# Kernel optimization log

Measured on AMD Instinct MI355X. Metric: run time of the kernel, lower is better.

## Reference

```python
import jax, jax.numpy as jnp
import numpy as np

B, T, H, W, C = 2, 8, 32, 32, 192
DI, N, K, DTR = 384, 16, 4, 12   # d_inner=2*dim, d_state, scan directions, dt_rank=ceil(dim/16)
LT, HID = 77, 768
L = T * H * W


def setup_inputs() -> dict:
    key = jax.random.key(0)
    ks = jax.random.split(key, 16)
    r = lambda i, shape, s=1.0: jax.random.normal(ks[i], shape, dtype=jnp.float32) * s
    return {
        "x": r(0, (B, T, H, W, C)),
        "text": r(1, (B, LT, C)),
        "cpe1_w": r(2, (C, 1, 3, 3, 3), 0.05), "cpe1_b": jnp.zeros((C,), jnp.float32),
        "cpe2_w": r(3, (C, 1, 3, 3, 3), 0.05), "cpe2_b": jnp.zeros((C,), jnp.float32),
        "norm1_g": jnp.ones((C,), jnp.float32), "norm1_b": jnp.zeros((C,), jnp.float32),
        "norm2_g": jnp.ones((C,), jnp.float32), "norm2_b": jnp.zeros((C,), jnp.float32),
        "in_proj_w": r(4, (2 * DI, C), 0.02), "in_proj_b": jnp.zeros((2 * DI,), jnp.float32),
        "text_proj_w": r(5, (DI, C), 0.02), "text_proj_b": jnp.zeros((DI,), jnp.float32),
        "conv_w": r(6, (DI, 1, 3, 3, 3), 0.05), "conv_b": jnp.zeros((DI,), jnp.float32),
        "x_proj_w": r(7, (K, DTR + 2 * N, DI), 0.02),
        "dt_proj_w": r(8, (K, DI, DTR), 0.1), "dt_proj_b": r(9, (K, DI), 0.1),
        "A_log": jnp.log(jnp.tile(jnp.arange(1.0, N + 1.0, dtype=jnp.float32)[None, None, :], (K, DI, 1))),
        "Ds": jnp.ones((K, DI), jnp.float32),
        "out_norm_g": jnp.ones((DI,), jnp.float32), "out_norm_b": jnp.zeros((DI,), jnp.float32),
        "out_proj_w": r(10, (C, DI), 0.02),
        "fc1_w": r(11, (HID, C), 0.02), "fc1_b": jnp.zeros((HID,), jnp.float32),
        "fc2_w": r(12, (C, HID), 0.02), "fc2_b": jnp.zeros((C,), jnp.float32),
    }


def _ln(x, g, b, eps=1e-6):
    m = x.mean(-1, keepdims=True)
    v = jnp.mean((x - m) ** 2, -1, keepdims=True)
    return (x - m) * jax.lax.rsqrt(v + eps) * g + b


def _dwconv3d(x, w, b):  # x [B, Ch, T, H, W], depthwise 3x3x3, SAME padding
    y = jax.lax.conv_general_dilated(x, w, (1, 1, 1), 'SAME',
                                     feature_group_count=x.shape[1],
                                     dimension_numbers=('NCDHW', 'OIDHW', 'NCDHW'))
    return y + b[None, :, None, None, None]


def _cpe(x, w, b):  # conv positional encoding, channels-last in/out
    return jnp.transpose(_dwconv3d(jnp.transpose(x, (0, 4, 1, 2, 3)), w, b), (0, 2, 3, 4, 1))


def _ss2d(x, text, p):
    # in-projection -> (x, z) gate split
    xz = x @ p['in_proj_w'].T + p['in_proj_b']           # [B,T,H,W,2*DI]
    xi, z = jnp.split(xz, 2, axis=-1)
    # text conditioning (pooled text tokens -> channel bias)
    cond = jax.nn.silu(text.mean(1) @ p['text_proj_w'].T + p['text_proj_b'])  # [B,DI]
    xi = xi + cond[:, None, None, None, :]
    # depthwise conv3d + SiLU
    xc = jax.nn.silu(_dwconv3d(jnp.transpose(xi, (0, 4, 1, 2, 3)), p['conv_w'], p['conv_b']))  # [B,DI,T,H,W]
    # cross-scan: (t,h,w), (t,w,h) and their reversals
    x0 = xc.reshape(B, DI, L)
    x1 = jnp.swapaxes(xc, 3, 4).reshape(B, DI, L)
    xs = jnp.stack([x0, x1, jnp.flip(x0, -1), jnp.flip(x1, -1)], 1)  # [B,K,DI,L]
    # per-direction projections
    xdbl = jnp.einsum('bkdl,kcd->bkcl', xs, p['x_proj_w'])
    dtr, Bm, Cm = jnp.split(xdbl, [DTR, DTR + N], axis=2)            # [B,K,DTR,L],[B,K,N,L],[B,K,N,L]
    dt = jax.nn.softplus(jnp.einsum('bkrl,kdr->bkdl', dtr, p['dt_proj_w']) + p['dt_proj_b'][None, :, :, None])
    A = -jnp.exp(p['A_log'])                                          # [K,DI,N]
    def step(h, inp):
        u_l, dt_l, B_l, C_l = inp
        h = h * jnp.exp(dt_l[..., None] * A) + (dt_l * u_l)[..., None] * B_l[:, :, None, :]
        return h, jnp.einsum('bkdn,bkn->bkd', h, C_l)
    seq = (xs.transpose(3, 0, 1, 2), dt.transpose(3, 0, 1, 2),
           Bm.transpose(3, 0, 1, 2), Cm.transpose(3, 0, 1, 2))
    _, ys = jax.lax.scan(step, jnp.zeros((B, K, DI, N), xs.dtype), seq)  # ys [L,B,K,DI]
    ys = ys.transpose(1, 2, 3, 0) + p['Ds'][None, :, :, None] * xs       # [B,K,DI,L]
    # merge the 4 directions back into (t,h,w) order
    unt = lambda y: jnp.swapaxes(y.reshape(B, DI, T, W, H), 3, 4).reshape(B, DI, L)
    y = ys[:, 0] + jnp.flip(ys[:, 2], -1) + unt(ys[:, 1]) + unt(jnp.flip(ys[:, 3], -1))
    y = _ln(y.transpose(0, 2, 1), p['out_norm_g'], p['out_norm_b']).reshape(B, T, H, W, DI)
    y = y * jax.nn.silu(z)
    return y @ p['out_proj_w'].T


def reference(x, text, cpe1_w, cpe1_b, cpe2_w, cpe2_b, norm1_g, norm1_b, norm2_g, norm2_b,
              in_proj_w, in_proj_b, text_proj_w, text_proj_b, conv_w, conv_b,
              x_proj_w, dt_proj_w, dt_proj_b, A_log, Ds, out_norm_g, out_norm_b, out_proj_w,
              fc1_w, fc1_b, fc2_w, fc2_b):
    p = dict(in_proj_w=in_proj_w, in_proj_b=in_proj_b, text_proj_w=text_proj_w,
             text_proj_b=text_proj_b, conv_w=conv_w, conv_b=conv_b, x_proj_w=x_proj_w,
             dt_proj_w=dt_proj_w, dt_proj_b=dt_proj_b, A_log=A_log, Ds=Ds,
             out_norm_g=out_norm_g, out_norm_b=out_norm_b, out_proj_w=out_proj_w)
    x = x + _cpe(x, cpe1_w, cpe1_b)
    x = x + _ss2d(_ln(x, norm1_g, norm1_b), text, p)
    x = x + _cpe(x, cpe2_w, cpe2_b)
    h = _ln(x, norm2_g, norm2_b)
    x = x + (jax.nn.gelu(h @ fc1_w.T + fc1_b) @ fc2_w.T + fc2_b)
    return x
```

## Files before the change

kernel.cpp:

```cpp
#include <hip/hip_runtime.h>
#include <hip/hip_bf16.h>

#define DEV __device__ __forceinline__

namespace {

constexpr int cB = 2, cT = 8, cH = 32, cW = 32, cC = 192;
constexpr int cDI = 384, cN = 16, cK = 4, cDTR = 12, cLT = 77, cHID = 768;
constexpr int cL  = cT * cH * cW;
constexpr int cBL = cB * cL;
constexpr int SEG = 128, SEGLEN = cL / SEG;
constexpr int XROW = cDTR + 2 * cN;
constexpr int XSTR = 48;

typedef __attribute__((ext_vector_type(8))) short bf16x8;
typedef __attribute__((ext_vector_type(4))) float f32x4;
typedef __attribute__((ext_vector_type(4))) short short4v;

DEV float bfu2f(unsigned short u) { return __uint_as_float(((unsigned)u) << 16); }
DEV float ldsel(const void* p, size_t i, int f32) {
  return f32 ? ((const float*)p)[i] : bfu2f(((const unsigned short*)p)[i]);
}
template <int F32>
DEV float4 ld4(const void* p, size_t e) {
  if (F32) return *(const float4*)((const float*)p + e);
  ushort4 u = *(const ushort4*)((const unsigned short*)p + e);
  return make_float4(bfu2f(u.x), bfu2f(u.y), bfu2f(u.z), bfu2f(u.w));
}
DEV short f2bf(float f) {
  unsigned u = __float_as_uint(f);
  u += 0x7fffu + ((u >> 16) & 1u);
  return (short)(u >> 16);
}
DEV float siluf(float x) { return x / (1.f + __expf(-x)); }
DEV float softplusf(float x) { return (x > 20.f) ? x : __logf(1.f + __expf(x)); }
DEV float gelut(float x) {
  float u = 0.7978845608028654f * (x + 0.044715f * x * x * x);
  float e = __expf(2.f * u);
  float th = 1.f - 2.f / (e + 1.f);
  return 0.5f * x * (1.f + th);
}

template <int BS>
DEV void blkreduce2(float& a, float& b) {
  __shared__ float ra[BS], rb[BS];
  int t = threadIdx.x;
  ra[t] = a; rb[t] = b; __syncthreads();
#pragma unroll
  for (int s = BS / 2; s > 0; s >>= 1) {
    if (t < s) { ra[t] += ra[t + s]; rb[t] += rb[t + s]; }
    __syncthreads();
  }
  a = ra[0]; b = rb[0];
  __syncthreads();
}

__global__ void __launch_bounds__(256) detect_kernel(
    const unsigned short* __restrict__ xa, const unsigned short* __restrict__ wp,
    int* __restrict__ flg) {
  __shared__ int cnt[2];
  if (threadIdx.x < 2) cnt[threadIdx.x] = 0;
  __syncthreads();
  int l0 = 0, l1 = 0;
  for (int i = threadIdx.x; i < 1024; i += 256) {
    float v = bfu2f(xa[2 * i]); float a = fabsf(v);
    if (v == 0.f || (a > 1e-8f && a < 1e4f)) l0++;
    float u = bfu2f(wp[2 * i]); float bq = fabsf(u);
    if (u == 0.f || (bq > 1e-8f && bq < 1e4f)) l1++;
  }
  atomicAdd(&cnt[0], l0); atomicAdd(&cnt[1], l1);
  __syncthreads();
  if (threadIdx.x == 0) {
    flg[0] = (cnt[0] < 614) ? 1 : 0;
    flg[1] = (cnt[1] < 614) ? 1 : 0;
    flg[2] = 1;
  }
}

__global__ void __launch_bounds__(256) prep_kernel(
    const void* __restrict__ cvw, const void* __restrict__ cvb,
    const void* __restrict__ c1w, const void* __restrict__ c1b,
    const void* __restrict__ c2w, const void* __restrict__ c2b,
    const int* __restrict__ flg,
    float* __restrict__ wcv, float* __restrict__ bcv,
    float* __restrict__ w1, float* __restrict__ b1,
    float* __restrict__ w2, float* __restrict__ b2) {
  int pf = flg[1];
  int i = blockIdx.x * 256 + threadIdx.x;
  int r = i;
  if (r < 27 * cDI) { int j = r / cDI, d = r % cDI; wcv[r] = ldsel(cvw, (size_t)d * 27 + j, pf); return; }
  r -= 27 * cDI;
  if (r < cDI) { bcv[r] = ldsel(cvb, r, pf); return; }
  r -= cDI;
  if (r < 27 * cC) { int j = r / cC, c = r % cC; w1[r] = ldsel(c1w, (size_t)c * 27 + j, pf); return; }
  r -= 27 * cC;
  if (r < cC) { b1[r] = ldsel(c1b, r, pf); return; }
  r -= cC;
  if (r < 27 * cC) { int j = r / cC, c = r % cC; w2[r] = ldsel(c2w, (size_t)c * 27 + j, pf); return; }
  r -= 27 * cC;
  if (r < cC) { b2[r] = ldsel(c2b, r, pf); return; }
}

template <int F32>
DEV void cpe_body(const void* __restrict__ xin, const float* __restrict__ wT,
                  const float* __restrict__ bs, int idx, float* __restrict__ out) {
  int c = (idx % (cC / 4)) * 4; int bv = idx / (cC / 4);
  int v = bv & (cL - 1); int b = bv >> 13;
  int t = v >> 10, q = v & 1023, h = q >> 5, w = q & 31;
  float4 acc = *(const float4*)(bs + c);
#pragma unroll
  for (int dz = 0; dz < 3; ++dz) {
    int tt = t + dz - 1; if ((unsigned)tt >= (unsigned)cT) continue;
#pragma unroll
    for (int dy = 0; dy < 3; ++dy) {
      int hh = h + dy - 1; if ((unsigned)hh >= (unsigned)cH) continue;
#pragma unroll
      for (int dx = 0; dx < 3; ++dx) {
        int ww = w + dx - 1; if ((unsigned)ww >= (unsigned)cW) continue;
        int vv = (tt << 10) + (hh << 5) + ww;
        float4 wv = *(const float4*)(wT + (dz * 9 + dy * 3 + dx) * cC + c);
        float4 xv = ld4<F32>(xin, ((size_t)b * cL + vv) * cC + c);
        acc.x += wv.x * xv.x; acc.y += wv.y * xv.y;
        acc.z += wv.z * xv.z; acc.w += wv.w * xv.w;
      }
    }
  }
  float4 x0 = ld4<F32>(xin, (size_t)bv * cC + c);
  float4 o = make_float4(x0.x + acc.x, x0.y + acc.y, x0.z + acc.z, x0.w + acc.w);
  *(float4*)(out + (size_t)bv * cC + c) = o;
}

__global__ void __launch_bounds__(256) cpe_kernel(
    const void* __restrict__ xin, const float* __restrict__ wT,
    const float* __restrict__ bs, const int* __restrict__ flg, int afidx,
    float* __restrict__ out) {
  int idx = blockIdx.x * 256 + threadIdx.x;
  if (idx >= cBL * cC / 4) return;
  if (flg[afidx]) cpe_body<1>(xin, wT, bs, idx, out);
  else            cpe_body<0>(xin, wT, bs, idx, out);
}

__global__ void __launch_bounds__(256) dwconv_silu_kernel(
    const float* __restrict__ xin, const float* __restrict__ wT,
    const float* __restrict__ bs, unsigned short* __restrict__ out) {
  int idx = blockIdx.x * 256 + threadIdx.x;
  if (idx >= cBL * cDI / 4) return;
  int d = (idx % (cDI / 4)) * 4; int bv = idx / (cDI / 4);
  int v = bv & (cL - 1); int b = bv >> 13;
  int t = v >> 10, q = v & 1023, h = q >> 5, w = q & 31;
  float4 acc = *(const float4*)(bs + d);
#pragma unroll
  for (int dz = 0; dz < 3; ++dz) {
    int tt = t + dz - 1; if ((unsigned)tt >= (unsigned)cT) continue;
#pragma unroll
    for (int dy = 0; dy < 3; ++dy) {
      int hh = h + dy - 1; if ((unsigned)hh >= (unsigned)cH) continue;
#pragma unroll
      for (int dx = 0; dx < 3; ++dx) {
        int ww = w + dx - 1; if ((unsigned)ww >= (unsigned)cW) continue;
        int vv = (tt << 10) + (hh << 5) + ww;
        float4 wv = *(const float4*)(wT + (dz * 9 + dy * 3 + dx) * cDI + d);
        float4 xv = *(const float4*)(xin + ((size_t)b * cL + vv) * cDI + d);
        acc.x += wv.x * xv.x; acc.y += wv.y * xv.y;
        acc.z += wv.z * xv.z; acc.w += wv.w * xv.w;
      }
    }
  }
  ushort4 o;
  o.x = (unsigned short)f2bf(siluf(acc.x));
  o.y = (unsigned short)f2bf(siluf(acc.y));
  o.z = (unsigned short)f2bf(siluf(acc.z));
  o.w = (unsigned short)f2bf(siluf(acc.w));
  *(ushort4*)(out + (size_t)bv * cDI + d) = o;
}

__global__ void __launch_bounds__(256) ln_kernel(
    const float* __restrict__ in, const void* __restrict__ g,
    const void* __restrict__ bb, const int* __restrict__ flg,
    float* __restrict__ out, int D) {
  int pf = flg[1];
  int row = blockIdx.x;
  const float* x = in + (size_t)row * D;
  float s1 = 0.f, s2 = 0.f;
  for (int i = threadIdx.x; i < D; i += 256) { float v = x[i]; s1 += v; s2 += v * v; }
  blkreduce2<256>(s1, s2);
  float mean = s1 / D;
  float var = s2 / D - mean * mean;
  float rstd = rsqrtf(var + 1e-6f);
  float* o = out + (size_t)row * D;
  for (int i = threadIdx.x; i < D; i += 256)
    o[i] = (x[i] - mean) * rstd * ldsel(g, i, pf) + ldsel(bb, i, pf);
}

__global__ void __launch_bounds__(384) text_cond_kernel(
    const void* __restrict__ text, const void* __restrict__ tw,
    const void* __restrict__ tb, const int* __restrict__ flg,
    float* __restrict__ cond) {
  int af = flg[0], pf = flg[1];
  __shared__ float mean[cC];
  int b = blockIdx.x;
  for (int c = threadIdx.x; c < cC; c += 384) {
    float s = 0.f;
    for (int t = 0; t < cLT; ++t) s += ldsel(text, ((size_t)b * cLT + t) * cC + c, af);
    mean[c] = s * (1.f / cLT);
  }
  __syncthreads();
  int di = threadIdx.x;
  float a = ldsel(tb, di, pf);
  for (int c = 0; c < cC; ++c) a += mean[c] * ldsel(tw, di * cC + c, pf);
  cond[b * cDI + di] = siluf(a);
}

template <int MODE, int ABF>
__global__ void __launch_bounds__(256) gemm_mfma_kernel(
    const void* __restrict__ A, const void* __restrict__ W,
    int N, int K, const void* __restrict__ bias, const int* __restrict__ flg,
    const float* __restrict__ extra, float* __restrict__ out,
    unsigned short* __restrict__ out2) {
  constexpr int BM = 128, BN = 64, BK = 32, PK = 40;
  __shared__ short As[BM * PK];
  __shared__ short Bs[BN * PK];
  int pf = flg[1];
  int tid = threadIdx.x;
  int m0 = blockIdx.y * BM, n0 = blockIdx.x * BN;
  int lane = tid & 63, wv = tid >> 6;
  int wm = (wv >> 1) * 64, wn = (wv & 1) * 32;
  int lr = lane & 15, quad = lane >> 4;
  f32x4 acc[4][2];
#pragma unroll
  for (int mi = 0; mi < 4; ++mi)
#pragma unroll
    for (int ni = 0; ni < 2; ++ni) { acc[mi][ni][0]=0.f; acc[mi][ni][1]=0.f; acc[mi][ni][2]=0.f; acc[mi][ni][3]=0.f; }
  int ar = tid >> 1, aks = (tid & 1) * 16;
  int wr = tid >> 2, wks = (tid & 3) * 8;
  for (int k0 = 0; k0 < K; k0 += BK) {
    if (ABF) {
      const unsigned short* ap = (const unsigned short*)A + (size_t)(m0 + ar) * K + k0 + aks;
      short* da = &As[ar * PK + aks];
#pragma unroll
      for (int i = 0; i < 4; ++i)
        *(short4v*)(da + i * 4) = *(const short4v*)(ap + i * 4);
    } else {
      const float* ap = (const float*)A + (size_t)(m0 + ar) * K + k0 + aks;
      short* da = &As[ar * PK + aks];
#pragma unroll
      for (int i = 0; i < 4; ++i) {
        float4 v = ((const float4*)ap)[i];
        short4v h; h.x = f2bf(v.x); h.y = f2bf(v.y); h.z = f2bf(v.z); h.w = f2bf(v.w);
        *(short4v*)(da + i * 4) = h;
      }
    }
    {
      int nr = n0 + wr;
      short hb[8];
      if (nr < N) {
        size_t wi = (size_t)nr * K + k0 + wks;
        if (pf) {
#pragma unroll
          for (int i = 0; i < 8; ++i) hb[i] = f2bf(((const float*)W)[wi + i]);
        } else {
#pragma unroll
          for (int i = 0; i < 8; ++i) hb[i] = (short)((const unsigned short*)W)[wi + i];
        }
      } else {
#pragma unroll
        for (int i = 0; i < 8; ++i) hb[i] = 0;
      }
      short* db = &Bs[wr * PK + wks];
#pragma unroll
      for (int i = 0; i < 8; i += 4) {
        short4v h; h.x = hb[i]; h.y = hb[i+1]; h.z = hb[i+2]; h.w = hb[i+3];
        *(short4v*)(db + i) = h;
      }
    }
    __syncthreads();
    bf16x8 af[4], bfr[2];
#pragma unroll
    for (int mi = 0; mi < 4; ++mi)
      af[mi] = *(const bf16x8*)&As[(wm + mi * 16 + lr) * PK + quad * 8];
#pragma unroll
    for (int ni = 0; ni < 2; ++ni)
      bfr[ni] = *(const bf16x8*)&Bs[(wn + ni * 16 + lr) * PK + quad * 8];
#pragma unroll
    for (int mi = 0; mi < 4; ++mi)
#pragma unroll
      for (int ni = 0; ni < 2; ++ni)
        acc[mi][ni] = __builtin_amdgcn_mfma_f32_16x16x32_bf16(af[mi], bfr[ni], acc[mi][ni], 0, 0, 0);
    __syncthreads();
  }
#pragma unroll
  for (int mi = 0; mi < 4; ++mi) {
#pragma unroll
    for (int ni = 0; ni < 2; ++ni) {
#pragma unroll
      for (int r = 0; r < 4; ++r) {
        int m = m0 + wm + mi * 16 + quad * 4 + r;
        int n = n0 + wn + ni * 16 + lr;
        float v = acc[mi][ni][r];
        if (MODE == 0) {
          float bvv = ldsel(bias, n, pf);
          int b = m >> 13;
          if (n < cDI) out[(size_t)m * cDI + n] = v + bvv + extra[b * cDI + n];
          else         out2[(size_t)m * cDI + (n - cDI)] = (unsigned short)f2bf(v + bvv);
        } else if (MODE == 1) {
          if (n < cK * XROW) {
            int k = n / XROW, c = n - k * XROW;
            int b = m >> 13, vv = m & (cL - 1);
            int t = vv >> 10, q = vv & 1023, h = q >> 5, w = q & 31;
            int l1 = (t << 10) + (w << 5) + h;
            int lk = (k == 0) ? vv : (k == 1) ? l1 : (k == 2) ? (cL - 1 - vv) : (cL - 1 - l1);
            out[((size_t)(b * cK + k) * cL + lk) * XSTR + c] = v;
          }
        } else if (MODE == 2) {
          out[(size_t)m * cC + n] = v + extra[(size_t)m * cC + n];
        } else if (MODE == 3) {
          out[(size_t)m * cHID + n] = gelut(v + ldsel(bias, n, pf));
        } else {
          out[(size_t)m * cC + n] = v + ldsel(bias, n, pf) + extra[(size_t)m * cC + n];
        }
      }
    }
  }
}

DEV int scan_voxel(int k, int l) {
  if (k == 0) return l;
  if (k == 2) return cL - 1 - l;
  int ll = (k == 1) ? l : (cL - 1 - l);
  int t = ll >> 10, q = ll & 1023, w = q >> 5, h = q & 31;
  return (t << 10) + (h << 5) + w;
}

struct Row11 { float4 r0, r1, r2, r3, r4, r5, r6, r7, r8, r9, r10; };
struct Row7  { float4 r0, r1, r2, r7, r8, r9, r10; };

DEV Row11 ldrow11(const float* __restrict__ rows, int st) {
  const float4* rp = (const float4*)(rows + st * XSTR);
  Row11 q;
  q.r0 = rp[0]; q.r1 = rp[1]; q.r2 = rp[2]; q.r3 = rp[3]; q.r4 = rp[4];
  q.r5 = rp[5]; q.r6 = rp[6]; q.r7 = rp[7]; q.r8 = rp[8]; q.r9 = rp[9];
  q.r10 = rp[10];
  return q;
}
DEV Row7 ldrow7(const float* __restrict__ rows, int st) {
  const float4* rp = (const float4*)(rows + st * XSTR);
  Row7 q;
  q.r0 = rp[0]; q.r1 = rp[1]; q.r2 = rp[2];
  q.r7 = rp[7]; q.r8 = rp[8]; q.r9 = rp[9]; q.r10 = rp[10];
  return q;
}

DEV float s1step(const Row11& q, float u,
                 const float (&wdt)[cDTR], float dtb, float ac0, float Dsd,
                 float (&h)[cN], float& P1) {
  float s0 = dtb + q.r0.x*wdt[0] + q.r0.z*wdt[2] + q.r1.x*wdt[4] + q.r1.z*wdt[6] + q.r2.x*wdt[8] + q.r2.z*wdt[10];
  float s1 = q.r0.y*wdt[1] + q.r0.w*wdt[3] + q.r1.y*wdt[5] + q.r1.w*wdt[7] + q.r2.y*wdt[9] + q.r2.w*wdt[11];
  float dt = softplusf(s0 + s1);
  float a1 = exp2f(dt * ac0);
  float a2 = a1*a1, a3 = a2*a1, a4 = a2*a2;
  float a5 = a4*a1, a6 = a4*a2, a7 = a4*a3, a8 = a4*a4;
  float a9 = a8*a1, a10 = a8*a2, a11 = a8*a3, a12 = a8*a4;
  float a13 = a8*a5, a14 = a8*a6, a15 = a8*a7, a16 = a8*a8;
  float dtu = dt * u;
  P1 *= a1;
  float yp0 = Dsd * u, yp1 = 0.f, yp2 = 0.f, yp3 = 0.f;
  h[0]  = h[0] *a1  + dtu*q.r3.x; yp0 += h[0] *q.r7.x;
  h[1]  = h[1] *a2  + dtu*q.r3.y; yp1 += h[1] *q.r7.y;
  h[2]  = h[2] *a3  + dtu*q.r3.z; yp2 += h[2] *q.r7.z;
  h[3]  = h[3] *a4  + dtu*q.r3.w; yp3 += h[3] *q.r7.w;
  h[4]  = h[4] *a5  + dtu*q.r4.x; yp0 += h[4] *q.r8.x;
  h[5]  = h[5] *a6  + dtu*q.r4.y; yp1 += h[5] *q.r8.y;
  h[6]  = h[6] *a7  + dtu*q.r4.z; yp2 += h[6] *q.r8.z;
  h[7]  = h[7] *a8  + dtu*q.r4.w; yp3 += h[7] *q.r8.w;
  h[8]  = h[8] *a9  + dtu*q.r5.x; yp0 += h[8] *q.r9.x;
  h[9]  = h[9] *a10 + dtu*q.r5.y; yp1 += h[9] *q.r9.y;
  h[10] = h[10]*a11 + dtu*q.r5.z; yp2 += h[10]*q.r9.z;
  h[11] = h[11]*a12 + dtu*q.r5.w; yp3 += h[11]*q.r9.w;
  h[12] = h[12]*a13 + dtu*q.r6.x; yp0 += h[12]*q.r10.x;
  h[13] = h[13]*a14 + dtu*q.r6.y; yp1 += h[13]*q.r10.y;
  h[14] = h[14]*a15 + dtu*q.r6.z; yp2 += h[14]*q.r10.z;
  h[15] = h[15]*a16 + dtu*q.r6.w; yp3 += h[15]*q.r10.w;
  return (yp0 + yp1) + (yp2 + yp3);
}

DEV float s3step(const Row7& q,
                 const float (&wdt)[cDTR], float dtb, float ac0,
                 float (&g)[cN]) {
  float s0 = dtb + q.r0.x*wdt[0] + q.r0.z*wdt[2] + q.r1.x*wdt[4] + q.r1.z*wdt[6] + q.r2.x*wdt[8] + q.r2.z*wdt[10];
  float s1 = q.r0.y*wdt[1] + q.r0.w*wdt[3] + q.r1.y*wdt[5] + q.r1.w*wdt[7] + q.r2.y*wdt[9] + q.r2.w*wdt[11];
  float dt = softplusf(s0 + s1);
  float a1 = exp2f(dt * ac0);
  float a2 = a1*a1, a3 = a2*a1, a4 = a2*a2;
  float a5 = a4*a1, a6 = a4*a2, a7 = a4*a3, a8 = a4*a4;
  float a9 = a8*a1, a10 = a8*a2, a11 = a8*a3, a12 = a8*a4;
  float a13 = a8*a5, a14 = a8*a6, a15 = a8*a7, a16 = a8*a8;
  float yp0 = 0.f, yp1 = 0.f, yp2 = 0.f, yp3 = 0.f;
  g[0]  *= a1;  yp0 += g[0] *q.r7.x;
  g[1]  *= a2;  yp1 += g[1] *q.r7.y;
  g[2]  *= a3;  yp2 += g[2] *q.r7.z;
  g[3]  *= a4;  yp3 += g[3] *q.r7.w;
  g[4]  *= a5;  yp0 += g[4] *q.r8.x;
  g[5]  *= a6;  yp1 += g[5] *q.r8.y;
  g[6]  *= a7;  yp2 += g[6] *q.r8.z;
  g[7]  *= a8;  yp3 += g[7] *q.r8.w;
  g[8]  *= a9;  yp0 += g[8] *q.r9.x;
  g[9]  *= a10; yp1 += g[9] *q.r9.y;
  g[10] *= a11; yp2 += g[10]*q.r9.z;
  g[11] *= a12; yp3 += g[11]*q.r9.w;
  g[12] *= a13; yp0 += g[12]*q.r10.x;
  g[13] *= a14; yp1 += g[13]*q.r10.y;
  g[14] *= a15; yp2 += g[14]*q.r10.z;
  g[15] *= a16; yp3 += g[15]*q.r10.w;
  return (yp0 + yp1) + (yp2 + yp3);
}

__global__ void __launch_bounds__(128, 3) scan1_kernel(
    const unsigned short* __restrict__ xch, const float* __restrict__ xdbl,
    const void* __restrict__ dtw, const void* __restrict__ dtbv,
    const void* __restrict__ alog, const void* __restrict__ dsv,
    const int* __restrict__ flg,
    unsigned short* __restrict__ ys0, unsigned short* __restrict__ ys1,
    unsigned short* __restrict__ ys2, unsigned short* __restrict__ ys3,
    unsigned short* __restrict__ hend, unsigned short* __restrict__ pend) {
  __shared__ float rows[SEGLEN * XSTR];
  int pf = flg[1];
  int tid = threadIdx.x;
  int d = blockIdx.x * 128 + tid;
  int bks = blockIdx.y;
  int s = bks & (SEG - 1); int bk = bks / SEG; int k = bk & 3; int b = bk >> 2;
  int l0 = s * SEGLEN;
  {
    const float4* src = (const float4*)(xdbl + ((size_t)bk * cL + l0) * XSTR);
    float4* dst = (float4*)rows;
#pragma unroll
    for (int i = 0; i < (SEGLEN * XSTR / 4) / 128; ++i)
      dst[tid + i * 128] = src[tid + i * 128];
  }
  float wdt[cDTR];
#pragma unroll
  for (int r = 0; r < cDTR; ++r) wdt[r] = ldsel(dtw, (size_t)(k * cDI + d) * cDTR + r, pf);
  float dtb = ldsel(dtbv, k * cDI + d, pf);
  float ac[cN];
#pragma unroll
  for (int n = 0; n < cN; ++n)
    ac[n] = -__expf(ldsel(alog, (size_t)(k * cDI + d) * cN + n, pf)) * 1.4426950408889634f;
  bool fast = true;
#pragma unroll
  for (int n = 1; n < cN; ++n)
    fast = fast && (fabsf(ac[n] - (float)(n + 1) * ac[0]) <= 1e-3f * fabsf(ac[n]));
  float Dsd = ldsel(dsv, k * cDI + d, pf);
  float h[cN];
#pragma unroll
  for (int n = 0; n < cN; ++n) h[n] = 0.f;
  size_t so = ((size_t)bks * cDI + d) * cN;
  const unsigned short* xcb = xch + (size_t)b * cL * cDI + d;
  unsigned short* ysk = (k == 0) ? ys0 : (k == 1) ? ys1 : (k == 2) ? ys2 : ys3;
  unsigned short* ysrow = ysk + ((size_t)b * cL + l0) * cDI + d;
  __syncthreads();
  if (fast) {
    float ac0 = ac[0];
    float P1 = 1.f;
    Row11 qa = ldrow11(rows, 0);
    float u0 = bfu2f(xcb[(size_t)scan_voxel(k, l0) * cDI]);
    float u1 = bfu2f(xcb[(size_t)scan_voxel(k, l0 + 1) * cDI]);
    for (int st = 0; st < SEGLEN; st += 2) {
      Row11 qb = ldrow11(rows, st + 1);
      int p2 = (st + 2 < SEGLEN) ? st + 2 : SEGLEN - 1;
      int p3 = (st + 3 < SEGLEN) ? st + 3 : SEGLEN - 1;
      float nu0 = bfu2f(xcb[(size_t)scan_voxel(k, l0 + p2) * cDI]);
      float nu1 = bfu2f(xcb[(size_t)scan_voxel(k, l0 + p3) * cDI]);
      float ya = s1step(qa, u0, wdt, dtb, ac0, Dsd, h, P1);
      ysrow[(size_t)st * cDI] = (unsigned short)f2bf(ya);
      qa = ldrow11(rows, p2);
      float yb = s1step(qb, u1, wdt, dtb, ac0, Dsd, h, P1);
      ysrow[(size_t)(st + 1) * cDI] = (unsigned short)f2bf(yb);
      u0 = nu0; u1 = nu1;
    }
    float pp = P1;
#pragma unroll
    for (int n = 0; n < cN; ++n) {
      hend[so + n] = (unsigned short)f2bf(h[n]);
      pend[so + n] = (unsigned short)f2bf(pp);
      pp *= P1;
    }
  } else {
    float P[cN];
#pragma unroll
    for (int n = 0; n < cN; ++n) P[n] = 1.f;
    for (int st = 0; st < SEGLEN; ++st) {
      int l = l0 + st;
      const float4* rp = (const float4*)(rows + st * XSTR);
      float4 q0 = rp[0], q1 = rp[1], q2 = rp[2];
      float s0 = dtb + q0.x*wdt[0] + q0.z*wdt[2] + q1.x*wdt[4] + q1.z*wdt[6] + q2.x*wdt[8] + q2.z*wdt[10];
      float s1 = q0.y*wdt[1] + q0.w*wdt[3] + q1.y*wdt[5] + q1.w*wdt[7] + q2.y*wdt[9] + q2.w*wdt[11];
      float dt = softplusf(s0 + s1);
      float Bv[cN], Cv[cN];
      float4 qb0 = rp[3], qb1 = rp[4], qb2 = rp[5], qb3 = rp[6];
      float4 qc0 = rp[7], qc1 = rp[8], qc2 = rp[9], qc3 = rp[10];
      Bv[0]=qb0.x; Bv[1]=qb0.y; Bv[2]=qb0.z; Bv[3]=qb0.w;
      Bv[4]=qb1.x; Bv[5]=qb1.y; Bv[6]=qb1.z; Bv[7]=qb1.w;
      Bv[8]=qb2.x; Bv[9]=qb2.y; Bv[10]=qb2.z; Bv[11]=qb2.w;
      Bv[12]=qb3.x; Bv[13]=qb3.y; Bv[14]=qb3.z; Bv[15]=qb3.w;
      Cv[0]=qc0.x; Cv[1]=qc0.y; Cv[2]=qc0.z; Cv[3]=qc0.w;
      Cv[4]=qc1.x; Cv[5]=qc1.y; Cv[6]=qc1.z; Cv[7]=qc1.w;
      Cv[8]=qc2.x; Cv[9]=qc2.y; Cv[10]=qc2.z; Cv[11]=qc2.w;
      Cv[12]=qc3.x; Cv[13]=qc3.y; Cv[14]=qc3.z; Cv[15]=qc3.w;
      int v = scan_voxel(k, l);
      float u = bfu2f(xcb[(size_t)v * cDI]);
      float dtu = dt * u;
      float y = Dsd * u;
#pragma unroll
      for (int n = 0; n < cN; ++n) {
        float a = exp2f(dt * ac[n]);
        h[n] = h[n] * a + dtu * Bv[n];
        P[n] *= a;
        y += h[n] * Cv[n];
      }
      ysrow[(size_t)st * cDI] = (unsigned short)f2bf(y);
    }
#pragma unroll
    for (int n = 0; n < cN; ++n) {
      hend[so + n] = (unsigned short)f2bf(h[n]);
      pend[so + n] = (unsigned short)f2bf(P[n]);
    }
  }
}

__global__ void __launch_bounds__(256) scan2_kernel(
    unsigned short* __restrict__ hend, const unsigned short* __restrict__ pend) {
  int tid = blockIdx.x * 256 + threadIdx.x;
  int bk = tid / (cDI * cN); int r = tid - bk * (cDI * cN);
  float g = 0.f;
  for (int s = 0; s < SEG; ++s) {
    size_t o = ((size_t)(bk * SEG + s) * cDI * cN) + r;
    float he = bfu2f(hend[o]), pe = bfu2f(pend[o]);
    hend[o] = (unsigned short)f2bf(g);
    g = pe * g + he;
  }
}

__global__ void __launch_bounds__(128, 3) scan3_kernel(
    const float* __restrict__ xdbl,
    const void* __restrict__ dtw, const void* __restrict__ dtbv,
    const void* __restrict__ alog, const int* __restrict__ flg,
    const unsigned short* __restrict__ hin,
    unsigned short* __restrict__ ys0, unsigned short* __restrict__ ys1,
    unsigned short* __restrict__ ys2, unsigned short* __restrict__ ys3) {
  int bks = blockIdx.y;
  int s = bks & (SEG - 1);
  if (s == 0) return;
  __shared__ float rows[SEGLEN * XSTR];
  int pf = flg[1];
  int tid = threadIdx.x;
  int d = blockIdx.x * 128 + tid;
  int bk = bks / SEG; int k = bk & 3; int b = bk >> 2;
  int l0 = s * SEGLEN;
  {
    const float4* src = (const float4*)(xdbl + ((size_t)bk * cL + l0) * XSTR);
    float4* dst = (float4*)rows;
#pragma unroll
    for (int i = 0; i < (SEGLEN * XSTR / 4) / 128; ++i)
      dst[tid + i * 128] = src[tid + i * 128];
  }
  float wdt[cDTR];
#pragma unroll
  for (int r = 0; r < cDTR; ++r) wdt[r] = ldsel(dtw, (size_t)(k * cDI + d) * cDTR + r, pf);
  float dtb = ldsel(dtbv, k * cDI + d, pf);
  float ac[cN];
#pragma unroll
  for (int n = 0; n < cN; ++n)
    ac[n] = -__expf(ldsel(alog, (size_t)(k * cDI + d) * cN + n, pf)) * 1.4426950408889634f;
  bool fast = true;
#pragma unroll
  for (int n = 1; n < cN; ++n)
    fast = fast && (fabsf(ac[n] - (float)(n + 1) * ac[0]) <= 1e-3f * fabsf(ac[n]));
  float g[cN];
  size_t so = ((size_t)bks * cDI + d) * cN;
#pragma unroll
  for (int n = 0; n < cN; ++n) g[n] = bfu2f(hin[so + n]);
  unsigned short* ysk = (k == 0) ? ys0 : (k == 1) ? ys1 : (k == 2) ? ys2 : ys3;
  unsigned short* ysrow = ysk + ((size_t)b * cL + l0) * cDI + d;
  __syncthreads();
  if (fast) {
    float ac0 = ac[0];
    Row7 qa = ldrow7(rows, 0);
    for (int st = 0; st < SEGLEN; st += 2) {
      Row7 qb = ldrow7(rows, st + 1);
      int p2 = (st + 2 < SEGLEN) ? st + 2 : SEGLEN - 1;
      float ya = s3step(qa, wdt, dtb, ac0, g);
      size_t ia = (size_t)st * cDI;
      ysrow[ia] = (unsigned short)f2bf(bfu2f(ysrow[ia]) + ya);
      qa = ldrow7(rows, p2);
      float yb = s3step(qb, wdt, dtb, ac0, g);
      size_t ib = (size_t)(st + 1) * cDI;
      ysrow[ib] = (unsigned short)f2bf(bfu2f(ysrow[ib]) + yb);
    }
  } else {
    for (int st = 0; st < SEGLEN; ++st) {
      const float4* rp = (const float4*)(rows + st * XSTR);
      float4 q0 = rp[0], q1 = rp[1], q2 = rp[2];
      float s0 = dtb + q0.x*wdt[0] + q0.z*wdt[2] + q1.x*wdt[4] + q1.z*wdt[6] + q2.x*wdt[8] + q2.z*wdt[10];
      float s1 = q0.y*wdt[1] + q0.w*wdt[3] + q1.y*wdt[5] + q1.w*wdt[7] + q2.y*wdt[9] + q2.w*wdt[11];
      float dt = softplusf(s0 + s1);
      float Cv[cN];
      float4 qc0 = rp[7], qc1 = rp[8], qc2 = rp[9], qc3 = rp[10];
      Cv[0]=qc0.x; Cv[1]=qc0.y; Cv[2]=qc0.z; Cv[3]=qc0.w;
      Cv[4]=qc1.x; Cv[5]=qc1.y; Cv[6]=qc1.z; Cv[7]=qc1.w;
      Cv[8]=qc2.x; Cv[9]=qc2.y; Cv[10]=qc2.z; Cv[11]=qc2.w;
      Cv[12]=qc3.x; Cv[13]=qc3.y; Cv[14]=qc3.z; Cv[15]=qc3.w;
      float y = 0.f;
#pragma unroll
      for (int n = 0; n < cN; ++n) {
        float a = exp2f(dt * ac[n]);
        g[n] *= a;
        y += g[n] * Cv[n];
      }
      size_t ii = (size_t)st * cDI;
      ysrow[ii] = (unsigned short)f2bf(bfu2f(ysrow[ii]) + y);
    }
  }
}

__global__ void __launch_bounds__(128) merge_kernel(
    const unsigned short* __restrict__ ys0, const unsigned short* __restrict__ ys1,
    const unsigned short* __restrict__ ys2, const unsigned short* __restrict__ ys3,
    const unsigned short* __restrict__ zh,
    const void* __restrict__ ong, const void* __restrict__ onb,
    const int* __restrict__ flg, unsigned short* __restrict__ yg) {
  int pf = flg[1];
  int bv = blockIdx.x;
  int v = bv & (cL - 1); int b = bv >> 13;
  int t = v >> 10, q = v & 1023, hh = q >> 5, ww = q & 31;
  int l1 = (t << 10) + (ww << 5) + hh;
  size_t r0 = ((size_t)b * cL + v) * cDI;
  size_t r1 = ((size_t)b * cL + l1) * cDI;
  size_t r2 = ((size_t)b * cL + (cL - 1 - v)) * cDI;
  size_t r3 = ((size_t)b * cL + (cL - 1 - l1)) * cDI;
  float vals[3]; float s1 = 0.f, s2 = 0.f;
#pragma unroll
  for (int i = 0; i < 3; ++i) {
    int d = threadIdx.x + i * 128;
    float x = bfu2f(ys0[r0 + d]) + bfu2f(ys1[r1 + d]) +
              bfu2f(ys2[r2 + d]) + bfu2f(ys3[r3 + d]);
    vals[i] = x; s1 += x; s2 += x * x;
  }
  blkreduce2<128>(s1, s2);
  float mean = s1 * (1.f / cDI);
  float var = s2 * (1.f / cDI) - mean * mean;
  float rstd = rsqrtf(var + 1e-6f);
  const unsigned short* zr = zh + (size_t)bv * cDI;
  unsigned short* og = yg + (size_t)bv * cDI;
#pragma unroll
  for (int i = 0; i < 3; ++i) {
    int d = threadIdx.x + i * 128;
    float xn = (vals[i] - mean) * rstd * ldsel(ong, d, pf) + ldsel(onb, d, pf);
    og[d] = (unsigned short)f2bf(xn * siluf(bfu2f(zr[d])));
  }
}

}

extern "C" void kernel_launch(void* const* d_in, const int* in_sizes, int n_in,
                              void* d_out, int out_size, void* d_ws, size_t ws_size,
                              hipStream_t stream) {
  (void)in_sizes; (void)n_in; (void)out_size; (void)ws_size;
  const void* x    = d_in[0];
  const void* text = d_in[1];
  const void* c1w  = d_in[2];
  const void* c1b  = d_in[3];
  const void* c2w  = d_in[4];
  const void* c2b  = d_in[5];
  const void* n1g  = d_in[6];
  const void* n1b  = d_in[7];
  const void* n2g  = d_in[8];
  const void* n2b  = d_in[9];
  const void* ipw  = d_in[10];
  const void* ipb  = d_in[11];
  const void* tpw  = d_in[12];
  const void* tpb  = d_in[13];
  const void* cvw  = d_in[14];
  const void* cvb  = d_in[15];
  const void* xpw  = d_in[16];
  const void* dtw  = d_in[17];
  const void* dtb  = d_in[18];
  const void* alog = d_in[19];
  const void* dsv  = d_in[20];
  const void* ong  = d_in[21];
  const void* onb  = d_in[22];
  const void* opw  = d_in[23];
  const void* f1w  = d_in[24];
  const void* f1b  = d_in[25];
  const void* f2w  = d_in[26];
  const void* f2b  = d_in[27];

  float* Wf = (float*)d_ws;

  constexpr size_t oC  = 0;
  constexpr size_t oD  = 6291456;
  constexpr size_t oG  = 9437184;
  constexpr size_t oA  = 12582912;
  constexpr size_t oB  = 18874368;
  constexpr size_t oE  = 25165824;
  constexpr size_t oF  = 28311552;
  constexpr size_t oCO = 31457280;
  constexpr size_t oFL = 31458048;
  constexpr size_t oWCV = 31458052;
  constexpr size_t oBCV = 31468420;
  constexpr size_t oW1  = 31468804;
  constexpr size_t oB1  = 31473988;
  constexpr size_t oW2  = 31474180;
  constexpr size_t oB2  = 31479364;
  unsigned short* xch = (unsigned short*)(Wf + oC);
  unsigned short* ysd2 = (unsigned short*)(Wf + oC + 3145728);
  float* xdbl = Wf + oD;
  unsigned short* ygh  = (unsigned short*)(Wf + oD);
  float* xn   = Wf + oG;
  unsigned short* pendp = (unsigned short*)(Wf + oG);
  unsigned short* ysd0 = (unsigned short*)(Wf + oA);
  unsigned short* ysd1 = (unsigned short*)(Wf + oA + 3145728);
  float* xi   = Wf + oA;
  float* x2   = Wf + oA;
  unsigned short* zh   = (unsigned short*)(Wf + oB);
  unsigned short* ysd3 = (unsigned short*)(Wf + oB + 3145728);
  float* x3   = Wf + oB;
  float* x1   = Wf + oE;
  unsigned short* hendp = (unsigned short*)(Wf + oF);
  float* xn2  = Wf + oF;
  float* cond = Wf + oCO;
  float* hbuf = Wf + oC;
  int*   flg  = (int*)(Wf + oFL);
  float* wcv = Wf + oWCV; float* bcv = Wf + oBCV;
  float* w1t = Wf + oW1;  float* b1t = Wf + oB1;
  float* w2t = Wf + oW2;  float* b2t = Wf + oB2;

  const int cpeBlocks = (cBL * cC / 4) / 256;
  const int dwBlocks  = (cBL * cDI / 4) / 256;

  hipLaunchKernelGGL(detect_kernel, dim3(1), dim3(256), 0, stream,
                     (const unsigned short*)x, (const unsigned short*)ipw, flg);
  hipLaunchKernelGGL(prep_kernel, dim3(85), dim3(256), 0, stream,
                     cvw, cvb, c1w, c1b, c2w, c2b, flg, wcv, bcv, w1t, b1t, w2t, b2t);
  hipLaunchKernelGGL(cpe_kernel, dim3(cpeBlocks), dim3(256), 0, stream,
                     x, w1t, b1t, flg, 0, x1);
  hipLaunchKernelGGL(ln_kernel, dim3(cBL), dim3(256), 0, stream, x1, n1g, n1b, flg, xn, cC);
  hipLaunchKernelGGL(text_cond_kernel, dim3(cB), dim3(384), 0, stream, text, tpw, tpb, flg, cond);
  hipLaunchKernelGGL((gemm_mfma_kernel<0, 0>), dim3(2 * cDI / 64, cBL / 128), dim3(256), 0, stream,
                     xn, ipw, 2 * cDI, cC, ipb, flg, cond, xi, zh);
  hipLaunchKernelGGL(dwconv_silu_kernel, dim3(dwBlocks), dim3(256), 0, stream,
                     xi, wcv, bcv, xch);
  hipLaunchKernelGGL((gemm_mfma_kernel<1, 1>), dim3((cK * XROW + 63) / 64, cBL / 128), dim3(256), 0, stream,
                     xch, xpw, cK * XROW, cDI, (const void*)nullptr, flg,
                     (const float*)nullptr, xdbl, (unsigned short*)nullptr);
  hipLaunchKernelGGL(scan1_kernel, dim3(cDI / 128, cB * cK * SEG), dim3(128), 0, stream,
                     xch, xdbl, dtw, dtb, alog, dsv, flg,
                     ysd0, ysd1, ysd2, ysd3, hendp, pendp);
  hipLaunchKernelGGL(scan2_kernel, dim3(cB * cK * cDI * cN / 256), dim3(256), 0, stream,
                     hendp, pendp);
  hipLaunchKernelGGL(scan3_kernel, dim3(cDI / 128, cB * cK * SEG), dim3(128), 0, stream,
                     xdbl, dtw, dtb, alog, flg, hendp, ysd0, ysd1, ysd2, ysd3);
  hipLaunchKernelGGL(merge_kernel, dim3(cBL), dim3(128), 0, stream,
                     ysd0, ysd1, ysd2, ysd3, zh, ong, onb, flg, ygh);
  hipLaunchKernelGGL((gemm_mfma_kernel<2, 1>), dim3(cC / 64, cBL / 128), dim3(256), 0, stream,
                     ygh, opw, cC, cDI, (const void*)nullptr, flg, x1, x2,
                     (unsigned short*)nullptr);
  hipLaunchKernelGGL(cpe_kernel, dim3(cpeBlocks), dim3(256), 0, stream,
                     x2, w2t, b2t, flg, 2, x3);
  hipLaunchKernelGGL(ln_kernel, dim3(cBL), dim3(256), 0, stream, x3, n2g, n2b, flg, xn2, cC);
  hipLaunchKernelGGL((gemm_mfma_kernel<3, 0>), dim3(cHID / 64, cBL / 128), dim3(256), 0, stream,
                     xn2, f1w, cHID, cC, f1b, flg, (const float*)nullptr, hbuf,
                     (unsigned short*)nullptr);
  hipLaunchKernelGGL((gemm_mfma_kernel<4, 0>), dim3(cC / 64, cBL / 128), dim3(256), 0, stream,
                     hbuf, f2w, cC, cHID, f2b, flg, x3, (float*)d_out,
                     (unsigned short*)nullptr);
}
```

Before: 638.3 us.

## Store intermediate activations in bf16 and use wave-per-row LayerNorm

The LayerNorm outputs, the in_proj x-branch, and the fc1 GELU output are now written as bf16 instead of fp32. The consuming GEMMs switch to their bf16 A-operand template variant, and the depthwise conv now reads bf16. This halves the memory traffic for these large intermediates and removes per-element conversion in the GEMM A loads. LayerNorm is rewritten to handle one row per 64-lane wave with shuffle reductions, four rows per block, replacing the 256-thread block reduction over 192 elements. The cost is extra bf16 rounding of intermediates, which slightly affects accuracy.

```diff
diff --git a/kernel.cpp b/kernel.cpp
--- a/kernel.cpp
+++ b/kernel.cpp
@@ -141,7 +141,7 @@
 }
 
 __global__ void __launch_bounds__(256) dwconv_silu_kernel(
-    const float* __restrict__ xin, const float* __restrict__ wT,
+    const unsigned short* __restrict__ xin, const float* __restrict__ wT,
     const float* __restrict__ bs, unsigned short* __restrict__ out) {
   int idx = blockIdx.x * 256 + threadIdx.x;
   if (idx >= cBL * cDI / 4) return;
@@ -160,9 +160,9 @@
         int ww = w + dx - 1; if ((unsigned)ww >= (unsigned)cW) continue;
         int vv = (tt << 10) + (hh << 5) + ww;
         float4 wv = *(const float4*)(wT + (dz * 9 + dy * 3 + dx) * cDI + d);
-        float4 xv = *(const float4*)(xin + ((size_t)b * cL + vv) * cDI + d);
-        acc.x += wv.x * xv.x; acc.y += wv.y * xv.y;
-        acc.z += wv.z * xv.z; acc.w += wv.w * xv.w;
+        ushort4 u4 = *(const ushort4*)(xin + ((size_t)b * cL + vv) * cDI + d);
+        acc.x += wv.x * bfu2f(u4.x); acc.y += wv.y * bfu2f(u4.y);
+        acc.z += wv.z * bfu2f(u4.z); acc.w += wv.w * bfu2f(u4.w);
       }
     }
   }
@@ -174,22 +174,29 @@
   *(ushort4*)(out + (size_t)bv * cDI + d) = o;
 }
 
-__global__ void __launch_bounds__(256) ln_kernel(
+__global__ void __launch_bounds__(256) lnb_kernel(
     const float* __restrict__ in, const void* __restrict__ g,
     const void* __restrict__ bb, const int* __restrict__ flg,
-    float* __restrict__ out, int D) {
+    unsigned short* __restrict__ out) {
   int pf = flg[1];
-  int row = blockIdx.x;
-  const float* x = in + (size_t)row * D;
-  float s1 = 0.f, s2 = 0.f;
-  for (int i = threadIdx.x; i < D; i += 256) { float v = x[i]; s1 += v; s2 += v * v; }
-  blkreduce2<256>(s1, s2);
-  float mean = s1 / D;
-  float var = s2 / D - mean * mean;
+  int row = blockIdx.x * 4 + (threadIdx.x >> 6);
+  int lane = threadIdx.x & 63;
+  const float* x = in + (size_t)row * cC;
+  float v0 = x[lane], v1 = x[lane + 64], v2 = x[lane + 128];
+  float s1 = v0 + v1 + v2;
+  float s2 = v0 * v0 + v1 * v1 + v2 * v2;
+#pragma unroll
+  for (int off = 32; off > 0; off >>= 1) {
+    s1 += __shfl_xor(s1, off);
+    s2 += __shfl_xor(s2, off);
+  }
+  float mean = s1 * (1.f / cC);
+  float var = s2 * (1.f / cC) - mean * mean;
   float rstd = rsqrtf(var + 1e-6f);
-  float* o = out + (size_t)row * D;
-  for (int i = threadIdx.x; i < D; i += 256)
-    o[i] = (x[i] - mean) * rstd * ldsel(g, i, pf) + ldsel(bb, i, pf);
+  unsigned short* o = out + (size_t)row * cC;
+  o[lane]       = (unsigned short)f2bf((v0 - mean) * rstd * ldsel(g, lane, pf)       + ldsel(bb, lane, pf));
+  o[lane + 64]  = (unsigned short)f2bf((v1 - mean) * rstd * ldsel(g, lane + 64, pf)  + ldsel(bb, lane + 64, pf));
+  o[lane + 128] = (unsigned short)f2bf((v2 - mean) * rstd * ldsel(g, lane + 128, pf) + ldsel(bb, lane + 128, pf));
 }
 
 __global__ void __launch_bounds__(384) text_cond_kernel(
@@ -300,8 +307,11 @@
         if (MODE == 0) {
           float bvv = ldsel(bias, n, pf);
           int b = m >> 13;
-          if (n < cDI) out[(size_t)m * cDI + n] = v + bvv + extra[b * cDI + n];
-          else         out2[(size_t)m * cDI + (n - cDI)] = (unsigned short)f2bf(v + bvv);
+          if (n < cDI)
+            ((unsigned short*)out)[(size_t)m * cDI + n] =
+                (unsigned short)f2bf(v + bvv + extra[b * cDI + n]);
+          else
+            out2[(size_t)m * cDI + (n - cDI)] = (unsigned short)f2bf(v + bvv);
         } else if (MODE == 1) {
           if (n < cK * XROW) {
             int k = n / XROW, c = n - k * XROW;
@@ -314,7 +324,8 @@
         } else if (MODE == 2) {
           out[(size_t)m * cC + n] = v + extra[(size_t)m * cC + n];
         } else if (MODE == 3) {
-          out[(size_t)m * cHID + n] = gelut(v + ldsel(bias, n, pf));
+          ((unsigned short*)out)[(size_t)m * cHID + n] =
+              (unsigned short)f2bf(gelut(v + ldsel(bias, n, pf)));
         } else {
           out[(size_t)m * cC + n] = v + ldsel(bias, n, pf) + extra[(size_t)m * cC + n];
         }
@@ -712,22 +723,22 @@
   constexpr size_t oB2  = 31479364;
   unsigned short* xch = (unsigned short*)(Wf + oC);
   unsigned short* ysd2 = (unsigned short*)(Wf + oC + 3145728);
+  unsigned short* hbufh = (unsigned short*)(Wf + oC);
   float* xdbl = Wf + oD;
   unsigned short* ygh  = (unsigned short*)(Wf + oD);
-  float* xn   = Wf + oG;
+  unsigned short* xnh  = (unsigned short*)(Wf + oG);
   unsigned short* pendp = (unsigned short*)(Wf + oG);
+  unsigned short* xib  = (unsigned short*)(Wf + oA);
   unsigned short* ysd0 = (unsigned short*)(Wf + oA);
   unsigned short* ysd1 = (unsigned short*)(Wf + oA + 3145728);
-  float* xi   = Wf + oA;
   float* x2   = Wf + oA;
   unsigned short* zh   = (unsigned short*)(Wf + oB);
   unsigned short* ysd3 = (unsigned short*)(Wf + oB + 3145728);
   float* x3   = Wf + oB;
   float* x1   = Wf + oE;
   unsigned short* hendp = (unsigned short*)(Wf + oF);
-  float* xn2  = Wf + oF;
+  unsigned short* xn2h = (unsigned short*)(Wf + oF);
   float* cond = Wf + oCO;
-  float* hbuf = Wf + oC;
   int*   flg  = (int*)(Wf + oFL);
   float* wcv = Wf + oWCV; float* bcv = Wf + oBCV;
   float* w1t = Wf + oW1;  float* b1t = Wf + oB1;
@@ -742,12 +753,12 @@
                      cvw, cvb, c1w, c1b, c2w, c2b, flg, wcv, bcv, w1t, b1t, w2t, b2t);
   hipLaunchKernelGGL(cpe_kernel, dim3(cpeBlocks), dim3(256), 0, stream,
                      x, w1t, b1t, flg, 0, x1);
-  hipLaunchKernelGGL(ln_kernel, dim3(cBL), dim3(256), 0, stream, x1, n1g, n1b, flg, xn, cC);
+  hipLaunchKernelGGL(lnb_kernel, dim3(cBL / 4), dim3(256), 0, stream, x1, n1g, n1b, flg, xnh);
   hipLaunchKernelGGL(text_cond_kernel, dim3(cB), dim3(384), 0, stream, text, tpw, tpb, flg, cond);
-  hipLaunchKernelGGL((gemm_mfma_kernel<0, 0>), dim3(2 * cDI / 64, cBL / 128), dim3(256), 0, stream,
-                     xn, ipw, 2 * cDI, cC, ipb, flg, cond, xi, zh);
+  hipLaunchKernelGGL((gemm_mfma_kernel<0, 1>), dim3(2 * cDI / 64, cBL / 128), dim3(256), 0, stream,
+                     xnh, ipw, 2 * cDI, cC, ipb, flg, cond, (float*)xib, zh);
   hipLaunchKernelGGL(dwconv_silu_kernel, dim3(dwBlocks), dim3(256), 0, stream,
-                     xi, wcv, bcv, xch);
+                     xib, wcv, bcv, xch);
   hipLaunchKernelGGL((gemm_mfma_kernel<1, 1>), dim3((cK * XROW + 63) / 64, cBL / 128), dim3(256), 0, stream,
                      xch, xpw, cK * XROW, cDI, (const void*)nullptr, flg,
                      (const float*)nullptr, xdbl, (unsigned short*)nullptr);
@@ -765,11 +776,11 @@
                      (unsigned short*)nullptr);
   hipLaunchKernelGGL(cpe_kernel, dim3(cpeBlocks), dim3(256), 0, stream,
                      x2, w2t, b2t, flg, 2, x3);
-  hipLaunchKernelGGL(ln_kernel, dim3(cBL), dim3(256), 0, stream, x3, n2g, n2b, flg, xn2, cC);
-  hipLaunchKernelGGL((gemm_mfma_kernel<3, 0>), dim3(cHID / 64, cBL / 128), dim3(256), 0, stream,
-                     xn2, f1w, cHID, cC, f1b, flg, (const float*)nullptr, hbuf,
+  hipLaunchKernelGGL(lnb_kernel, dim3(cBL / 4), dim3(256), 0, stream, x3, n2g, n2b, flg, xn2h);
+  hipLaunchKernelGGL((gemm_mfma_kernel<3, 1>), dim3(cHID / 64, cBL / 128), dim3(256), 0, stream,
+                     xn2h, f1w, cHID, cC, f1b, flg, (const float*)nullptr, (float*)hbufh,
                      (unsigned short*)nullptr);
-  hipLaunchKernelGGL((gemm_mfma_kernel<4, 0>), dim3(cC / 64, cBL / 128), dim3(256), 0, stream,
-                     hbuf, f2w, cC, cHID, f2b, flg, x3, (float*)d_out,
+  hipLaunchKernelGGL((gemm_mfma_kernel<4, 1>), dim3(cC / 64, cBL / 128), dim3(256), 0, stream,
+                     hbufh, f2w, cC, cHID, f2b, flg, x3, (float*)d_out,
                      (unsigned short*)nullptr);
 }
```

Result: faster. 616.6 us (-3.4%).
